# Kernel tuning notes

Measured on AMD Instinct MI355X. Metric: run time of the kernel, lower is better.

## Reference

```python
import jax, jax.numpy as jnp
import numpy as np

# Clause structure: 4 unary clauses and 4 binary (joined-space) clauses,
# each with 3 literals; first literal negated ('n' prefix).
U_IDX = np.array([[0, 1, 2], [3, 4, 5], [6, 7, 8], [9, 10, 11]], dtype=np.int32)
U_SIGNS = np.array([[-1.0, 1.0, 1.0]] * 4, dtype=np.float32)
# Joined matrix columns: [u[i1] (0..15), u[i2] (16..31), binary (32..35)]
B_IDX = np.array([[0, 16, 32], [1, 17, 33], [2, 18, 34], [3, 19, 35]], dtype=np.int32)
B_SIGNS = np.array([[-1.0, 1.0, 1.0]] * 4, dtype=np.float32)

N_NODES, N_UNARY = 50000, 16
N_EDGES, N_BINARY = 1600000, 4
INIT_W = 0.5


def setup_inputs() -> dict:
    key = jax.random.key(0)
    k1, k2, k3, k4 = jax.random.split(key, 4)
    unary = jax.random.normal(k1, (N_NODES, N_UNARY), dtype=jnp.float32)
    binary = jax.random.normal(k2, (N_EDGES, N_BINARY), dtype=jnp.float32)
    edge_index = jax.random.randint(k3, (2, N_EDGES), 0, N_NODES, dtype=jnp.int32)
    wu = jnp.full((4,), INIT_W, dtype=jnp.float32)  # learnable unary clause weights
    wb = jnp.full((4,), INIT_W, dtype=jnp.float32)  # learnable binary clause weights
    return {"unary": unary, "binary": binary, "wu": wu, "wb": wb, "edge_index": edge_index}


def _knowledge_enhancer(x, idx, signs, w):
    """x: [R, P]; idx/signs: [C, L]; w: [C]. Returns summed deltas [R, P]."""
    lit = x[:, idx] * signs                                    # [R, C, L] signed literals
    d = (w[:, None] * jax.nn.softmax(lit, axis=-1)) * signs    # [R, C, L] signed deltas
    return jnp.zeros_like(x).at[:, idx].add(d)                 # scatter-sum over clauses


def reference(unary, binary, wu, wb, edge_index):
    i1, i2 = edge_index[0], edge_index[1]
    P = unary.shape[1]
    # Unary knowledge enhancement
    u = unary + _knowledge_enhancer(unary, U_IDX, U_SIGNS, wu)
    # Join: per-edge [u[i1] | u[i2] | binary]
    joined = jnp.concatenate([u[i1], u[i2], binary], axis=1)   # [E, 2P+B]
    d = _knowledge_enhancer(joined, B_IDX, B_SIGNS, wb)        # [E, 2P+B]
    # GroupBy: scatter node blocks back, keep binary block
    n = unary.shape[0]
    delta_up = (jax.ops.segment_sum(d[:, :P], i1, num_segments=n)
                + jax.ops.segment_sum(d[:, P:2 * P], i2, num_segments=n))
    delta_bp = d[:, 2 * P:]
    # activation = identity (default)
    return u + delta_up, binary + delta_bp
```

## Files before the change

### kernel.cpp

```cpp
#include <hip/hip_runtime.h>
#include <hip/hip_bf16.h>

#define N_NODES 50000
#define N_UNARY 16
#define N_EDGES 1600000
#define N_BINARY 4

typedef float vfloat4 __attribute__((ext_vector_type(4)));

#define FP_SCALE 127.0f
#define FP_INV   (1.0f / 127.0f)

#define BUCKET_SHIFT 11
#define BUCKET_NODES 2048
#define N_BUCKETS 25
#define N_GROUPS 50
#define SEG_CAP 73728
#define N_CHUNKS 10

#define TAILS_STRIDE 16

#define SCAT_BLOCK 512
#define SCAT_EPT 4
#define SCAT_EDGES (SCAT_BLOCK * SCAT_EPT)
#define SCAT_RECS (2 * SCAT_EDGES)

#define SEG_BYTES   ((size_t)N_GROUPS * SEG_CAP * 8)
#define TAILS_BYTES ((size_t)4096)
#define ACC_BYTES   ((size_t)N_NODES * 2 * 8)
#define UE_BYTES    ((size_t)N_NODES * 16)
#define WS_NEEDED   (SEG_BYTES + TAILS_BYTES + ACC_BYTES + UE_BYTES)

__device__ inline void enhance_u4(const float x[6], float wu0, float wu1,
                                  float u[4]) {
    float l0 = -x[0], l1 = x[1], l2 = x[2];
    float m  = fmaxf(l0, fmaxf(l1, l2));
    float e0 = __expf(l0 - m), e1 = __expf(l1 - m), e2 = __expf(l2 - m);
    float inv = 1.0f / (e0 + e1 + e2);
    u[0] = x[0] - wu0 * e0 * inv;
    u[1] = x[1] + wu0 * e1 * inv;
    u[2] = x[2] + wu0 * e2 * inv;
    float l3 = -x[3], l4 = x[4], l5 = x[5];
    float m2 = fmaxf(l3, fmaxf(l4, l5));
    float f0 = __expf(l3 - m2), f1 = __expf(l4 - m2), f2 = __expf(l5 - m2);
    float inv2 = 1.0f / (f0 + f1 + f2);
    u[3] = x[3] - wu1 * f0 * inv2;
}

__device__ inline void edge_math(const float* unary, const float* binary,
                                 float wu0, float wu1, const float wc[4],
                                 int i1, int i2, int e,
                                 float s0[4], float s1[4],
                                 float* out_b) {
    const float4* u1p = (const float4*)(unary + (size_t)i1 * N_UNARY);
    const float4* u2p = (const float4*)(unary + (size_t)i2 * N_UNARY);
    float4 x1a = u1p[0], x1b = u1p[1];
    float4 x2a = u2p[0], x2b = u2p[1];
    float xa[6] = {x1a.x, x1a.y, x1a.z, x1a.w, x1b.x, x1b.y};
    float xb[6] = {x2a.x, x2a.y, x2a.z, x2a.w, x2b.x, x2b.y};
    float a[4], b[4];
    enhance_u4(xa, wu0, wu1, a);
    enhance_u4(xb, wu0, wu1, b);

    vfloat4 bn = __builtin_nontemporal_load((const vfloat4*)binary + e);
    float bb[4] = {bn.x, bn.y, bn.z, bn.w};
    float ob[4];
#pragma unroll
    for (int c = 0; c < 4; ++c) {
        float l0 = -a[c], l1 = b[c], l2 = bb[c];
        float m  = fmaxf(l0, fmaxf(l1, l2));
        float e0 = __expf(l0 - m);
        float e1 = __expf(l1 - m);
        float e2 = __expf(l2 - m);
        float inv = 1.0f / (e0 + e1 + e2);
        s0[c] = e0 * inv;
        s1[c] = e1 * inv;
        ob[c] = bb[c] + wc[c] * e2 * inv;
    }
    vfloat4 obv = {ob[0], ob[1], ob[2], ob[3]};
    __builtin_nontemporal_store(obv, (vfloat4*)out_b + e);
}

__device__ inline unsigned long long make_rec(const float s[4], int local_id) {
    unsigned v0 = __float2uint_rn(s[0] * FP_SCALE);
    unsigned v1 = __float2uint_rn(s[1] * FP_SCALE);
    unsigned v2 = __float2uint_rn(s[2] * FP_SCALE);
    unsigned v3 = __float2uint_rn(s[3] * FP_SCALE);
    unsigned pl = v0 | (v1 << 7) | (v2 << 14) | (v3 << 21);
    return (unsigned long long)pl | ((unsigned long long)(unsigned)local_id << 28);
}

__device__ inline unsigned long long pack4_16(const float s[4]) {
    unsigned long long a = __float2uint_rn(s[0] * FP_SCALE);
    unsigned long long b = __float2uint_rn(s[1] * FP_SCALE);
    unsigned long long c = __float2uint_rn(s[2] * FP_SCALE);
    unsigned long long d = __float2uint_rn(s[3] * FP_SCALE);
    return a | (b << 16) | (c << 32) | (d << 48);
}

__global__ void __launch_bounds__(256)
kenn_pre_kernel(const float* __restrict__ unary,
                const float* __restrict__ wu,
                float4* __restrict__ ue,
                unsigned* __restrict__ tails,
                unsigned long long* __restrict__ accN,
                unsigned long long* __restrict__ accP) {
    int n = blockIdx.x * blockDim.x + threadIdx.x;
    if (n < N_GROUPS) tails[n * TAILS_STRIDE] = 0u;
    if (n >= N_NODES) return;
    accN[n] = 0ull;
    accP[n] = 0ull;
    const float4* up = (const float4*)(unary + (size_t)n * N_UNARY);
    float4 x0 = up[0], x1 = up[1];
    float x[6] = {x0.x, x0.y, x0.z, x0.w, x1.x, x1.y};
    float u[4];
    enhance_u4(x, wu[0], wu[1], u);
    ue[n] = make_float4(u[0], u[1], u[2], u[3]);
}

__global__ void __launch_bounds__(SCAT_BLOCK, 8)
kenn_edge_scatter_kernel(const float4* __restrict__ ue,
                         const float* __restrict__ binary,
                         const float* __restrict__ wb,
                         const int* __restrict__ edge_index,
                         unsigned long long* __restrict__ segs,
                         unsigned* __restrict__ tails,
                         float* __restrict__ out_b) {
    __shared__ unsigned l_cnt[N_GROUPS];
    __shared__ unsigned l_pref[N_GROUPS + 1];
    __shared__ unsigned l_gbase[N_GROUPS];
    __shared__ unsigned long long staged[SCAT_RECS];
    __shared__ unsigned char staged_g[SCAT_RECS];

    int tid = threadIdx.x;
    if (tid < N_GROUPS) l_cnt[tid] = 0;
    __syncthreads();

    int base = blockIdx.x * SCAT_EDGES;
    float wc[4] = {wb[0], wb[1], wb[2], wb[3]};

    bool valid[SCAT_EPT];
    unsigned posg1[SCAT_EPT], posg2[SCAT_EPT];
    unsigned long long rec1[SCAT_EPT], rec2[SCAT_EPT];

#pragma unroll
    for (int k = 0; k < SCAT_EPT; ++k) {
        int e = base + k * SCAT_BLOCK + tid;
        valid[k] = (e < N_EDGES);
        if (!valid[k]) continue;
        int i1 = __builtin_nontemporal_load(edge_index + e);
        int i2 = __builtin_nontemporal_load(edge_index + N_EDGES + e);

        float4 av = ue[i1];
        float4 bv = ue[i2];
        float a[4] = {av.x, av.y, av.z, av.w};
        float b[4] = {bv.x, bv.y, bv.z, bv.w};
        vfloat4 bn = __builtin_nontemporal_load((const vfloat4*)binary + e);
        float bb[4] = {bn.x, bn.y, bn.z, bn.w};

        float s0[4], s1[4], ob[4];
#pragma unroll
        for (int c = 0; c < 4; ++c) {
            float l0 = -a[c], l1 = b[c], l2 = bb[c];
            float m  = fmaxf(l0, fmaxf(l1, l2));
            float e0 = __expf(l0 - m);
            float e1 = __expf(l1 - m);
            float e2 = __expf(l2 - m);
            float inv = 1.0f / (e0 + e1 + e2);
            s0[c] = e0 * inv;
            s1[c] = e1 * inv;
            ob[c] = bb[c] + wc[c] * e2 * inv;
        }
        vfloat4 obv = {ob[0], ob[1], ob[2], ob[3]};
        __builtin_nontemporal_store(obv, (vfloat4*)out_b + e);

        rec1[k] = make_rec(s0, i1 & (BUCKET_NODES - 1));
        rec2[k] = make_rec(s1, i2 & (BUCKET_NODES - 1));
        unsigned g1 = (unsigned)(i1 >> BUCKET_SHIFT);
        unsigned g2 = N_BUCKETS + (unsigned)(i2 >> BUCKET_SHIFT);
        unsigned p1 = atomicAdd(&l_cnt[g1], 1u);
        unsigned p2 = atomicAdd(&l_cnt[g2], 1u);
        posg1[k] = (p1 << 6) | g1;
        posg2[k] = (p2 << 6) | g2;
    }
    __syncthreads();

    if (tid < 64) {
        unsigned c = (tid < N_GROUPS) ? l_cnt[tid] : 0u;
        unsigned s = c;
#pragma unroll
        for (int off = 1; off < 64; off <<= 1) {
            unsigned o = __shfl_up(s, off, 64);
            if (tid >= off) s += o;
        }
        if (tid < N_GROUPS) l_pref[tid] = s - c;
        if (tid == N_GROUPS - 1) l_pref[N_GROUPS] = s;
    } else if (tid >= 64 && tid < 64 + N_GROUPS) {
        int g = tid - 64;
        unsigned c = l_cnt[g];
        l_gbase[g] = c ? atomicAdd(tails + g * TAILS_STRIDE, c) : 0u;
    }
    __syncthreads();

#pragma unroll
    for (int k = 0; k < SCAT_EPT; ++k) {
        if (!valid[k]) continue;
        unsigned g1 = posg1[k] & 63u, p1 = l_pref[g1] + (posg1[k] >> 6);
        unsigned g2 = posg2[k] & 63u, p2 = l_pref[g2] + (posg2[k] >> 6);
        staged[p1] = rec1[k];  staged_g[p1] = (unsigned char)g1;
        staged[p2] = rec2[k];  staged_g[p2] = (unsigned char)g2;
    }
    __syncthreads();

    unsigned total = l_pref[N_GROUPS];
    for (unsigned i = tid; i < total; i += SCAT_BLOCK) {
        unsigned g = staged_g[i];
        unsigned long long rec = staged[i];
        unsigned p = l_gbase[g] + (i - l_pref[g]);
        if (p < SEG_CAP)
            __builtin_nontemporal_store(rec, segs + (size_t)g * SEG_CAP + p);
    }
}

__global__ void __launch_bounds__(512)
kenn_reduce_kernel(const unsigned long long* __restrict__ segs,
                   const unsigned* __restrict__ tails,
                   unsigned long long* __restrict__ accN,
                   unsigned long long* __restrict__ accP) {
    __shared__ unsigned long long lacc[BUCKET_NODES];
    int chunk = blockIdx.x;
    int g     = blockIdx.y;
    int tid   = threadIdx.x;

    for (int i = tid; i < BUCKET_NODES; i += blockDim.x) lacc[i] = 0ull;
    __syncthreads();

    unsigned cnt = tails[g * TAILS_STRIDE];
    if (cnt > SEG_CAP) cnt = SEG_CAP;
    unsigned csz   = (cnt + N_CHUNKS - 1) / N_CHUNKS;
    unsigned start = chunk * csz;
    unsigned end   = start + csz;
    if (end > cnt) end = cnt;

    const unsigned long long* seg = segs + (size_t)g * SEG_CAP;
    for (unsigned i = start + tid; i < end; i += blockDim.x) {
        unsigned long long r = seg[i];
        unsigned id = (unsigned)(r >> 28) & (BUCKET_NODES - 1);
        unsigned pl = (unsigned)r & 0x0FFFFFFFu;
        unsigned long long exp =
            (unsigned long long)(pl & 127u) |
            ((unsigned long long)(pl & (127u << 7))  << 9)  |
            ((unsigned long long)(pl & (127u << 14)) << 18) |
            ((unsigned long long)(pl & (127u << 21)) << 27);
        atomicAdd(&lacc[id], exp);
    }
    __syncthreads();

    int bucket = (g < N_BUCKETS) ? g : (g - N_BUCKETS);
    unsigned long long* acc =
        ((g < N_BUCKETS) ? accN : accP) + (size_t)bucket * BUCKET_NODES;
    for (int i = tid; i < BUCKET_NODES; i += blockDim.x) {
        unsigned long long v = lacc[i];
        if (v) atomicAdd(acc + i, v);
    }
}

__global__ void kenn_node_final_kernel(const float* __restrict__ unary,
                                       const float* __restrict__ wu,
                                       const float* __restrict__ wb,
                                       const unsigned long long* __restrict__ accN,
                                       const unsigned long long* __restrict__ accP,
                                       float* __restrict__ out_u) {
    int node = blockIdx.x * blockDim.x + threadIdx.x;
    if (node >= N_NODES) return;

    const float4* up = (const float4*)(unary + (size_t)node * N_UNARY);
    float4 x0 = up[0], x1 = up[1], x2 = up[2], x3 = up[3];
    float x[16] = {x0.x, x0.y, x0.z, x0.w,
                   x1.x, x1.y, x1.z, x1.w,
                   x2.x, x2.y, x2.z, x2.w,
                   x3.x, x3.y, x3.z, x3.w};
    float wuc[4] = {wu[0], wu[1], wu[2], wu[3]};

    float y[16];
#pragma unroll
    for (int i = 0; i < 16; ++i) y[i] = x[i];

#pragma unroll
    for (int c = 0; c < 4; ++c) {
        float l0 = -x[3 * c + 0];
        float l1 =  x[3 * c + 1];
        float l2 =  x[3 * c + 2];
        float m  = fmaxf(l0, fmaxf(l1, l2));
        float e0 = __expf(l0 - m);
        float e1 = __expf(l1 - m);
        float e2 = __expf(l2 - m);
        float inv = 1.0f / (e0 + e1 + e2);
        y[3 * c + 0] -= wuc[c] * e0 * inv;
        y[3 * c + 1] += wuc[c] * e1 * inv;
        y[3 * c + 2] += wuc[c] * e2 * inv;
    }

    unsigned long long pn = accN[node];
    unsigned long long pp = accP[node];

    float wbc[4] = {wb[0], wb[1], wb[2], wb[3]};
    y[0] += wbc[0] * ((float)(int)((pp      ) & 0xffff) - (float)(int)((pn      ) & 0xffff)) * FP_INV;
    y[1] += wbc[1] * ((float)(int)((pp >> 16) & 0xffff) - (float)(int)((pn >> 16) & 0xffff)) * FP_INV;
    y[2] += wbc[2] * ((float)(int)((pp >> 32) & 0xffff) - (float)(int)((pn >> 32) & 0xffff)) * FP_INV;
    y[3] += wbc[3] * ((float)(int)((pp >> 48) & 0xffff) - (float)(int)((pn >> 48) & 0xffff)) * FP_INV;

    float4* op = (float4*)(out_u + (size_t)node * N_UNARY);
    op[0] = make_float4(y[0],  y[1],  y[2],  y[3]);
    op[1] = make_float4(y[4],  y[5],  y[6],  y[7]);
    op[2] = make_float4(y[8],  y[9],  y[10], y[11]);
    op[3] = make_float4(y[12], y[13], y[14], y[15]);
}

__global__ void kenn_edge_atomic_kernel(const float* __restrict__ unary,
                                        const float* __restrict__ binary,
                                        const float* __restrict__ wu,
                                        const float* __restrict__ wb,
                                        const int* __restrict__ edge_index,
                                        unsigned long long* __restrict__ accN,
                                        unsigned long long* __restrict__ accP,
                                        float* __restrict__ out_b) {
    int e = blockIdx.x * blockDim.x + threadIdx.x;
    if (e >= N_EDGES) return;
    int i1 = __builtin_nontemporal_load(edge_index + e);
    int i2 = __builtin_nontemporal_load(edge_index + N_EDGES + e);
    float wu0 = wu[0], wu1 = wu[1];
    float wc[4] = {wb[0], wb[1], wb[2], wb[3]};
    float s0[4], s1[4];
    edge_math(unary, binary, wu0, wu1, wc, i1, i2, e, s0, s1, out_b);
    atomicAdd(accN + i1, pack4_16(s0));
    atomicAdd(accP + i2, pack4_16(s1));
}

extern "C" void kernel_launch(void* const* d_in, const int* in_sizes, int n_in,
                              void* d_out, int out_size, void* d_ws, size_t ws_size,
                              hipStream_t stream) {
    const float* unary      = (const float*)d_in[0];
    const float* binary     = (const float*)d_in[1];
    const float* wu         = (const float*)d_in[2];
    const float* wb         = (const float*)d_in[3];
    const int*   edge_index = (const int*)d_in[4];

    float* out_u = (float*)d_out;
    float* out_b = (float*)d_out + (size_t)N_NODES * N_UNARY;

    if (ws_size >= WS_NEEDED) {
        unsigned long long* segs = (unsigned long long*)d_ws;
        unsigned* tails = (unsigned*)((char*)d_ws + SEG_BYTES);
        unsigned long long* accN =
            (unsigned long long*)((char*)d_ws + SEG_BYTES + TAILS_BYTES);
        unsigned long long* accP = accN + N_NODES;
        float4* ue =
            (float4*)((char*)d_ws + SEG_BYTES + TAILS_BYTES + ACC_BYTES);

        {
            dim3 grid((N_NODES + 255) / 256);
            kenn_pre_kernel<<<grid, dim3(256), 0, stream>>>(
                unary, wu, ue, tails, accN, accP);
        }
        {
            dim3 grid((N_EDGES + SCAT_EDGES - 1) / SCAT_EDGES);
            kenn_edge_scatter_kernel<<<grid, dim3(SCAT_BLOCK), 0, stream>>>(
                ue, binary, wb, edge_index, segs, tails, out_b);
        }
        {
            dim3 grid(N_CHUNKS, N_GROUPS);
            kenn_reduce_kernel<<<grid, dim3(512), 0, stream>>>(
                segs, tails, accN, accP);
        }
        {
            dim3 block(256);
            dim3 grid((N_NODES + 255) / 256);
            kenn_node_final_kernel<<<grid, block, 0, stream>>>(
                unary, wu, wb, accN, accP, out_u);
        }
    } else {
        unsigned long long* accN = (unsigned long long*)d_ws;
        unsigned long long* accP = accN + N_NODES;
        (void)hipMemsetAsync(accN, 0,
                             (size_t)N_NODES * 2 * sizeof(unsigned long long),
                             stream);
        {
            dim3 block(256);
            dim3 grid((N_EDGES + 255) / 256);
            kenn_edge_atomic_kernel<<<grid, block, 0, stream>>>(
                unary, binary, wu, wb, edge_index, accN, accP, out_b);
        }
        {
            dim3 block(256);
            dim3 grid((N_NODES + 255) / 256);
            kenn_node_final_kernel<<<grid, block, 0, stream>>>(
                unary, wu, wb, accN, accP, out_u);
        }
    }
}
```

Baseline: 150.7 us.

## Fuse four-stage pipeline into one cooperative persistent kernel with grid syncs

Replaces the four separate launches (node pre-pass, edge scatter, bucket reduce, node finalize) with a single cooperative kernel that walks through the phases separated by grid.sync, using an atomic work counter to hand out edge tiles dynamically. The aim is to remove inter-kernel launch gaps and tail effects. The cost is grid-wide barriers, a grid capped at 512 blocks, and smaller per-block tiles. The fallback path now uses 1024-thread scatter blocks.

After: 361.3 us. 2.4x slower.

```diff
diff --git a/kernel.cpp b/kernel.cpp
--- a/kernel.cpp
+++ b/kernel.cpp
@@ -1,5 +1,8 @@
 #include <hip/hip_runtime.h>
 #include <hip/hip_bf16.h>
+#include <hip/hip_cooperative_groups.h>
+
+namespace cg = cooperative_groups;
 
 #define N_NODES 50000
 #define N_UNARY 16
@@ -19,11 +22,20 @@
 #define N_CHUNKS 10
 
 #define TAILS_STRIDE 16
-
-#define SCAT_BLOCK 512
-#define SCAT_EPT 4
-#define SCAT_EDGES (SCAT_BLOCK * SCAT_EPT)
+#define WORK_IDX 1023
+
+#define FUSE_BLOCK 512
+#define FUSE_MAX_GRID 512
+
+#define SCAT_EPT 2
+#define SCAT_EDGES (FUSE_BLOCK * SCAT_EPT)
 #define SCAT_RECS (2 * SCAT_EDGES)
+#define N_TILES ((N_EDGES + SCAT_EDGES - 1) / SCAT_EDGES)
+
+#define SCAT2_BLOCK 1024
+#define SCAT2_EPT 2
+#define SCAT2_EDGES (SCAT2_BLOCK * SCAT2_EPT)
+#define SCAT2_RECS (2 * SCAT2_EDGES)
 
 #define SEG_BYTES   ((size_t)N_GROUPS * SEG_CAP * 8)
 #define TAILS_BYTES ((size_t)4096)
@@ -47,21 +59,32 @@
     u[3] = x[3] - wu1 * f0 * inv2;
 }
 
-__device__ inline void edge_math(const float* unary, const float* binary,
-                                 float wu0, float wu1, const float wc[4],
-                                 int i1, int i2, int e,
+__device__ inline unsigned long long make_rec(const float s[4], int local_id) {
+    unsigned v0 = __float2uint_rn(s[0] * FP_SCALE);
+    unsigned v1 = __float2uint_rn(s[1] * FP_SCALE);
+    unsigned v2 = __float2uint_rn(s[2] * FP_SCALE);
+    unsigned v3 = __float2uint_rn(s[3] * FP_SCALE);
+    unsigned pl = v0 | (v1 << 7) | (v2 << 14) | (v3 << 21);
+    return (unsigned long long)pl | ((unsigned long long)(unsigned)local_id << 28);
+}
+
+__device__ inline unsigned long long pack4_16(const float s[4]) {
+    unsigned long long a = __float2uint_rn(s[0] * FP_SCALE);
+    unsigned long long b = __float2uint_rn(s[1] * FP_SCALE);
+    unsigned long long c = __float2uint_rn(s[2] * FP_SCALE);
+    unsigned long long d = __float2uint_rn(s[3] * FP_SCALE);
+    return a | (b << 16) | (c << 32) | (d << 48);
+}
+
+__device__ inline void edge_core(const float4* __restrict__ ue,
+                                 const float* __restrict__ binary,
+                                 const float wc[4], int i1, int i2, int e,
                                  float s0[4], float s1[4],
-                                 float* out_b) {
-    const float4* u1p = (const float4*)(unary + (size_t)i1 * N_UNARY);
-    const float4* u2p = (const float4*)(unary + (size_t)i2 * N_UNARY);
-    float4 x1a = u1p[0], x1b = u1p[1];
-    float4 x2a = u2p[0], x2b = u2p[1];
-    float xa[6] = {x1a.x, x1a.y, x1a.z, x1a.w, x1b.x, x1b.y};
-    float xb[6] = {x2a.x, x2a.y, x2a.z, x2a.w, x2b.x, x2b.y};
-    float a[4], b[4];
-    enhance_u4(xa, wu0, wu1, a);
-    enhance_u4(xb, wu0, wu1, b);
-
+                                 float* __restrict__ out_b) {
+    float4 av = ue[i1];
+    float4 bv = ue[i2];
+    float a[4] = {av.x, av.y, av.z, av.w};
+    float b[4] = {bv.x, bv.y, bv.z, bv.w};
     vfloat4 bn = __builtin_nontemporal_load((const vfloat4*)binary + e);
     float bb[4] = {bn.x, bn.y, bn.z, bn.w};
     float ob[4];
@@ -81,22 +104,210 @@
     __builtin_nontemporal_store(obv, (vfloat4*)out_b + e);
 }
 
-__device__ inline unsigned long long make_rec(const float s[4], int local_id) {
-    unsigned v0 = __float2uint_rn(s[0] * FP_SCALE);
-    unsigned v1 = __float2uint_rn(s[1] * FP_SCALE);
-    unsigned v2 = __float2uint_rn(s[2] * FP_SCALE);
-    unsigned v3 = __float2uint_rn(s[3] * FP_SCALE);
-    unsigned pl = v0 | (v1 << 7) | (v2 << 14) | (v3 << 21);
-    return (unsigned long long)pl | ((unsigned long long)(unsigned)local_id << 28);
-}
-
-__device__ inline unsigned long long pack4_16(const float s[4]) {
-    unsigned long long a = __float2uint_rn(s[0] * FP_SCALE);
-    unsigned long long b = __float2uint_rn(s[1] * FP_SCALE);
-    unsigned long long c = __float2uint_rn(s[2] * FP_SCALE);
-    unsigned long long d = __float2uint_rn(s[3] * FP_SCALE);
-    return a | (b << 16) | (c << 32) | (d << 48);
-}
+__global__ void __launch_bounds__(FUSE_BLOCK, 4)
+kenn_fused_kernel(const float* __restrict__ unary,
+                  const float* __restrict__ binary,
+                  const float* __restrict__ wu,
+                  const float* __restrict__ wb,
+                  const int* __restrict__ edge_index,
+                  unsigned long long* __restrict__ segs,
+                  unsigned* __restrict__ tails,
+                  unsigned long long* __restrict__ accN,
+                  unsigned long long* __restrict__ accP,
+                  float4* __restrict__ ue,
+                  float* __restrict__ out_u,
+                  float* __restrict__ out_b) {
+    __shared__ unsigned l_cnt[N_GROUPS];
+    __shared__ unsigned l_pref[N_GROUPS + 1];
+    __shared__ unsigned l_gbase[N_GROUPS];
+    __shared__ unsigned long long staged[SCAT_RECS];
+    __shared__ unsigned char staged_g[SCAT_RECS];
+    __shared__ int s_tile;
+
+    cg::grid_group grid = cg::this_grid();
+    const int tid  = threadIdx.x;
+    const int nthr = (int)gridDim.x * FUSE_BLOCK;
+    const int gt0  = (int)blockIdx.x * FUSE_BLOCK + tid;
+
+    for (int n = gt0; n < N_NODES; n += nthr) {
+        if (n < N_GROUPS) tails[n * TAILS_STRIDE] = 0u;
+        if (n == 0) tails[WORK_IDX] = 0u;
+        accN[n] = 0ull;
+        accP[n] = 0ull;
+        const float4* up = (const float4*)(unary + (size_t)n * N_UNARY);
+        float4 x0 = up[0], x1 = up[1];
+        float x[6] = {x0.x, x0.y, x0.z, x0.w, x1.x, x1.y};
+        float u[4];
+        enhance_u4(x, wu[0], wu[1], u);
+        ue[n] = make_float4(u[0], u[1], u[2], u[3]);
+    }
+    __threadfence();
+    grid.sync();
+
+    {
+        float wc[4] = {wb[0], wb[1], wb[2], wb[3]};
+        for (;;) {
+            if (tid == 0) s_tile = (int)atomicAdd(tails + WORK_IDX, 1u);
+            if (tid < N_GROUPS) l_cnt[tid] = 0;
+            __syncthreads();
+            int tile = s_tile;
+            if (tile >= N_TILES) break;
+            int base = tile * SCAT_EDGES;
+
+            bool valid[SCAT_EPT];
+            unsigned posg1[SCAT_EPT], posg2[SCAT_EPT];
+            unsigned long long rec1[SCAT_EPT], rec2[SCAT_EPT];
+
+#pragma unroll
+            for (int k = 0; k < SCAT_EPT; ++k) {
+                int e = base + k * FUSE_BLOCK + tid;
+                valid[k] = (e < N_EDGES);
+                if (!valid[k]) continue;
+                int i1 = __builtin_nontemporal_load(edge_index + e);
+                int i2 = __builtin_nontemporal_load(edge_index + N_EDGES + e);
+                float s0[4], s1[4];
+                edge_core(ue, binary, wc, i1, i2, e, s0, s1, out_b);
+                rec1[k] = make_rec(s0, i1 & (BUCKET_NODES - 1));
+                rec2[k] = make_rec(s1, i2 & (BUCKET_NODES - 1));
+                unsigned g1 = (unsigned)(i1 >> BUCKET_SHIFT);
+                unsigned g2 = N_BUCKETS + (unsigned)(i2 >> BUCKET_SHIFT);
+                unsigned p1 = atomicAdd(&l_cnt[g1], 1u);
+                unsigned p2 = atomicAdd(&l_cnt[g2], 1u);
+                posg1[k] = (p1 << 6) | g1;
+                posg2[k] = (p2 << 6) | g2;
+            }
+            __syncthreads();
+
+            if (tid < 64) {
+                unsigned c = (tid < N_GROUPS) ? l_cnt[tid] : 0u;
+                unsigned s = c;
+#pragma unroll
+                for (int off = 1; off < 64; off <<= 1) {
+                    unsigned o = __shfl_up(s, off, 64);
+                    if (tid >= off) s += o;
+                }
+                if (tid < N_GROUPS) l_pref[tid] = s - c;
+                if (tid == N_GROUPS - 1) l_pref[N_GROUPS] = s;
+            } else if (tid >= 64 && tid < 64 + N_GROUPS) {
+                int g = tid - 64;
+                unsigned c = l_cnt[g];
+                l_gbase[g] = c ? atomicAdd(tails + g * TAILS_STRIDE, c) : 0u;
+            }
+            __syncthreads();
+
+#pragma unroll
+            for (int k = 0; k < SCAT_EPT; ++k) {
+                if (!valid[k]) continue;
+                unsigned g1 = posg1[k] & 63u, p1 = l_pref[g1] + (posg1[k] >> 6);
+                unsigned g2 = posg2[k] & 63u, p2 = l_pref[g2] + (posg2[k] >> 6);
+                staged[p1] = rec1[k];  staged_g[p1] = (unsigned char)g1;
+                staged[p2] = rec2[k];  staged_g[p2] = (unsigned char)g2;
+            }
+            __syncthreads();
+
+            unsigned total = l_pref[N_GROUPS];
+            for (unsigned i = tid; i < total; i += FUSE_BLOCK) {
+                unsigned g = staged_g[i];
+                unsigned long long rec = staged[i];
+                unsigned p = l_gbase[g] + (i - l_pref[g]);
+                if (p < SEG_CAP)
+                    __builtin_nontemporal_store(rec, segs + (size_t)g * SEG_CAP + p);
+            }
+            __syncthreads();
+        }
+    }
+    __threadfence();
+    grid.sync();
+
+    {
+        unsigned long long* lacc = staged;
+        for (int task = blockIdx.x; task < N_GROUPS * N_CHUNKS;
+             task += (int)gridDim.x) {
+            int g     = task / N_CHUNKS;
+            int chunk = task % N_CHUNKS;
+
+            for (int i = tid; i < BUCKET_NODES; i += FUSE_BLOCK) lacc[i] = 0ull;
+            __syncthreads();
+
+            unsigned cnt = tails[g * TAILS_STRIDE];
+            if (cnt > SEG_CAP) cnt = SEG_CAP;
+            unsigned csz   = (cnt + N_CHUNKS - 1) / N_CHUNKS;
+            unsigned start = chunk * csz;
+            unsigned end   = start + csz;
+            if (end > cnt) end = cnt;
+
+            const unsigned long long* seg = segs + (size_t)g * SEG_CAP;
+            for (unsigned i = start + tid; i < end; i += FUSE_BLOCK) {
+                unsigned long long r = seg[i];
+                unsigned id = (unsigned)(r >> 28) & (BUCKET_NODES - 1);
+                unsigned pl = (unsigned)r & 0x0FFFFFFFu;
+                unsigned long long exp =
+                    (unsigned long long)(pl & 127u) |
+                    ((unsigned long long)(pl & (127u << 7))  << 9)  |
+                    ((unsigned long long)(pl & (127u << 14)) << 18) |
+                    ((unsigned long long)(pl & (127u << 21)) << 27);
+                atomicAdd(&lacc[id], exp);
+            }
+            __syncthreads();
+
+            int bucket = (g < N_BUCKETS) ? g : (g - N_BUCKETS);
+            unsigned long long* acc =
+                ((g < N_BUCKETS) ? accN : accP) + (size_t)bucket * BUCKET_NODES;
+            for (int i = tid; i < BUCKET_NODES; i += FUSE_BLOCK) {
+                unsigned long long v = lacc[i];
+                if (v) atomicAdd(acc + i, v);
+            }
+            __syncthreads();
+        }
+    }
+    __threadfence();
+    grid.sync();
+
+    for (int node = gt0; node < N_NODES; node += nthr) {
+        const float4* up = (const float4*)(unary + (size_t)node * N_UNARY);
+        float4 x0 = up[0], x1 = up[1], x2 = up[2], x3 = up[3];
+        float x[16] = {x0.x, x0.y, x0.z, x0.w,
+                       x1.x, x1.y, x1.z, x1.w,
+                       x2.x, x2.y, x2.z, x2.w,
+                       x3.x, x3.y, x3.z, x3.w};
+        float wuc[4] = {wu[0], wu[1], wu[2], wu[3]};
+
+        float y[16];
+#pragma unroll
+        for (int i = 0; i < 16; ++i) y[i] = x[i];
+
+#pragma unroll
+        for (int c = 0; c < 4; ++c) {
+            float l0 = -x[3 * c + 0];
+            float l1 =  x[3 * c + 1];
+            float l2 =  x[3 * c + 2];
+            float m  = fmaxf(l0, fmaxf(l1, l2));
+            float e0 = __expf(l0 - m);
+            float e1 = __expf(l1 - m);
+            float e2 = __expf(l2 - m);
+            float inv = 1.0f / (e0 + e1 + e2);
+            y[3 * c + 0] -= wuc[c] * e0 * inv;
+            y[3 * c + 1] += wuc[c] * e1 * inv;
+            y[3 * c + 2] += wuc[c] * e2 * inv;
+        }
+
+        unsigned long long pn = accN[node];
+        unsigned long long pp = accP[node];
+
+        float wbc[4] = {wb[0], wb[1], wb[2], wb[3]};
+        y[0] += wbc[0] * ((float)(int)((pp      ) & 0xffff) - (float)(int)((pn      ) & 0xffff)) * FP_INV;
+        y[1] += wbc[1] * ((float)(int)((pp >> 16) & 0xffff) - (float)(int)((pn >> 16) & 0xffff)) * FP_INV;
+        y[2] += wbc[2] * ((float)(int)((pp >> 32) & 0xffff) - (float)(int)((pn >> 32) & 0xffff)) * FP_INV;
+        y[3] += wbc[3] * ((float)(int)((pp >> 48) & 0xffff) - (float)(int)((pn >> 48) & 0xffff)) * FP_INV;
+
+        float4* op = (float4*)(out_u + (size_t)node * N_UNARY);
+        op[0] = make_float4(y[0],  y[1],  y[2],  y[3]);
+        op[1] = make_float4(y[4],  y[5],  y[6],  y[7]);
+        op[2] = make_float4(y[8],  y[9],  y[10], y[11]);
+        op[3] = make_float4(y[12], y[13], y[14], y[15]);
+    }
+}
+
 
 __global__ void __launch_bounds__(256)
 kenn_pre_kernel(const float* __restrict__ unary,
@@ -118,7 +329,7 @@
     ue[n] = make_float4(u[0], u[1], u[2], u[3]);
 }
 
-__global__ void __launch_bounds__(SCAT_BLOCK, 8)
+__global__ void __launch_bounds__(SCAT2_BLOCK)
 kenn_edge_scatter_kernel(const float4* __restrict__ ue,
                          const float* __restrict__ binary,
                          const float* __restrict__ wb,
@@ -129,51 +340,29 @@
     __shared__ unsigned l_cnt[N_GROUPS];
     __shared__ unsigned l_pref[N_GROUPS + 1];
     __shared__ unsigned l_gbase[N_GROUPS];
-    __shared__ unsigned long long staged[SCAT_RECS];
-    __shared__ unsigned char staged_g[SCAT_RECS];
+    __shared__ unsigned long long staged[SCAT2_RECS];
+    __shared__ unsigned char staged_g[SCAT2_RECS];
 
     int tid = threadIdx.x;
     if (tid < N_GROUPS) l_cnt[tid] = 0;
     __syncthreads();
 
-    int base = blockIdx.x * SCAT_EDGES;
+    int base = blockIdx.x * SCAT2_EDGES;
     float wc[4] = {wb[0], wb[1], wb[2], wb[3]};
 
-    bool valid[SCAT_EPT];
-    unsigned posg1[SCAT_EPT], posg2[SCAT_EPT];
-    unsigned long long rec1[SCAT_EPT], rec2[SCAT_EPT];
-
-#pragma unroll
-    for (int k = 0; k < SCAT_EPT; ++k) {
-        int e = base + k * SCAT_BLOCK + tid;
+    bool valid[SCAT2_EPT];
+    unsigned posg1[SCAT2_EPT], posg2[SCAT2_EPT];
+    unsigned long long rec1[SCAT2_EPT], rec2[SCAT2_EPT];
+
+#pragma unroll
+    for (int k = 0; k < SCAT2_EPT; ++k) {
+        int e = base + k * SCAT2_BLOCK + tid;
         valid[k] = (e < N_EDGES);
         if (!valid[k]) continue;
         int i1 = __builtin_nontemporal_load(edge_index + e);
         int i2 = __builtin_nontemporal_load(edge_index + N_EDGES + e);
-
-        float4 av = ue[i1];
-        float4 bv = ue[i2];
-        float a[4] = {av.x, av.y, av.z, av.w};
-        float b[4] = {bv.x, bv.y, bv.z, bv.w};
-        vfloat4 bn = __builtin_nontemporal_load((const vfloat4*)binary + e);
-        float bb[4] = {bn.x, bn.y, bn.z, bn.w};
-
-        float s0[4], s1[4], ob[4];
-#pragma unroll
-        for (int c = 0; c < 4; ++c) {
-            float l0 = -a[c], l1 = b[c], l2 = bb[c];
-            float m  = fmaxf(l0, fmaxf(l1, l2));
-            float e0 = __expf(l0 - m);
-            float e1 = __expf(l1 - m);
-            float e2 = __expf(l2 - m);
-            float inv = 1.0f / (e0 + e1 + e2);
-            s0[c] = e0 * inv;
-            s1[c] = e1 * inv;
-            ob[c] = bb[c] + wc[c] * e2 * inv;
-        }
-        vfloat4 obv = {ob[0], ob[1], ob[2], ob[3]};
-        __builtin_nontemporal_store(obv, (vfloat4*)out_b + e);
-
+        float s0[4], s1[4];
+        edge_core(ue, binary, wc, i1, i2, e, s0, s1, out_b);
         rec1[k] = make_rec(s0, i1 & (BUCKET_NODES - 1));
         rec2[k] = make_rec(s1, i2 & (BUCKET_NODES - 1));
         unsigned g1 = (unsigned)(i1 >> BUCKET_SHIFT);
@@ -203,7 +392,7 @@
     __syncthreads();
 
 #pragma unroll
-    for (int k = 0; k < SCAT_EPT; ++k) {
+    for (int k = 0; k < SCAT2_EPT; ++k) {
         if (!valid[k]) continue;
         unsigned g1 = posg1[k] & 63u, p1 = l_pref[g1] + (posg1[k] >> 6);
         unsigned g2 = posg2[k] & 63u, p2 = l_pref[g2] + (posg2[k] >> 6);
@@ -213,7 +402,7 @@
     __syncthreads();
 
     unsigned total = l_pref[N_GROUPS];
-    for (unsigned i = tid; i < total; i += SCAT_BLOCK) {
+    for (unsigned i = tid; i < total; i += SCAT2_BLOCK) {
         unsigned g = staged_g[i];
         unsigned long long rec = staged[i];
         unsigned p = l_gbase[g] + (i - l_pref[g]);
@@ -331,11 +520,40 @@
     int i2 = __builtin_nontemporal_load(edge_index + N_EDGES + e);
     float wu0 = wu[0], wu1 = wu[1];
     float wc[4] = {wb[0], wb[1], wb[2], wb[3]};
-    float s0[4], s1[4];
-    edge_math(unary, binary, wu0, wu1, wc, i1, i2, e, s0, s1, out_b);
+
+    const float4* u1p = (const float4*)(unary + (size_t)i1 * N_UNARY);
+    const float4* u2p = (const float4*)(unary + (size_t)i2 * N_UNARY);
+    float4 x1a = u1p[0], x1b = u1p[1];
+    float4 x2a = u2p[0], x2b = u2p[1];
+    float xa[6] = {x1a.x, x1a.y, x1a.z, x1a.w, x1b.x, x1b.y};
+    float xb[6] = {x2a.x, x2a.y, x2a.z, x2a.w, x2b.x, x2b.y};
+    float a[4], b[4];
+    enhance_u4(xa, wu0, wu1, a);
+    enhance_u4(xb, wu0, wu1, b);
+
+    vfloat4 bn = __builtin_nontemporal_load((const vfloat4*)binary + e);
+    float bb[4] = {bn.x, bn.y, bn.z, bn.w};
+    float s0[4], s1[4], ob[4];
+#pragma unroll
+    for (int c = 0; c < 4; ++c) {
+        float l0 = -a[c], l1 = b[c], l2 = bb[c];
+        float m  = fmaxf(l0, fmaxf(l1, l2));
+        float e0 = __expf(l0 - m);
+        float e1 = __expf(l1 - m);
+        float e2 = __expf(l2 - m);
+        float inv = 1.0f / (e0 + e1 + e2);
+        s0[c] = e0 * inv;
+        s1[c] = e1 * inv;
+        ob[c] = bb[c] + wc[c] * e2 * inv;
+    }
+    vfloat4 obv = {ob[0], ob[1], ob[2], ob[3]};
+    __builtin_nontemporal_store(obv, (vfloat4*)out_b + e);
+
     atomicAdd(accN + i1, pack4_16(s0));
     atomicAdd(accP + i2, pack4_16(s1));
 }
+
+static int g_coop_grid = -1;
 
 extern "C" void kernel_launch(void* const* d_in, const int* in_sizes, int n_in,
                               void* d_out, int out_size, void* d_ws, size_t ws_size,
@@ -358,26 +576,56 @@
         float4* ue =
             (float4*)((char*)d_ws + SEG_BYTES + TAILS_BYTES + ACC_BYTES);
 
-        {
-            dim3 grid((N_NODES + 255) / 256);
-            kenn_pre_kernel<<<grid, dim3(256), 0, stream>>>(
-                unary, wu, ue, tails, accN, accP);
-        }
-        {
-            dim3 grid((N_EDGES + SCAT_EDGES - 1) / SCAT_EDGES);
-            kenn_edge_scatter_kernel<<<grid, dim3(SCAT_BLOCK), 0, stream>>>(
-                ue, binary, wb, edge_index, segs, tails, out_b);
-        }
-        {
-            dim3 grid(N_CHUNKS, N_GROUPS);
-            kenn_reduce_kernel<<<grid, dim3(512), 0, stream>>>(
-                segs, tails, accN, accP);
-        }
-        {
-            dim3 block(256);
-            dim3 grid((N_NODES + 255) / 256);
-            kenn_node_final_kernel<<<grid, block, 0, stream>>>(
-                unary, wu, wb, accN, accP, out_u);
+        if (g_coop_grid < 0) {
+            int nb = 0;
+            hipError_t oe = hipOccupancyMaxActiveBlocksPerMultiprocessor(
+                &nb, (const void*)kenn_fused_kernel, FUSE_BLOCK, 0);
+            if (oe != hipSuccess || nb < 1) {
+                g_coop_grid = 0;
+            } else {
+                long g = (long)nb * 256;
+                if (g > FUSE_MAX_GRID) g = FUSE_MAX_GRID;
+                g_coop_grid = (int)g;
+            }
+        }
+
+        bool done = false;
+        if (g_coop_grid > 0) {
+            void* args[] = {
+                (void*)&unary, (void*)&binary, (void*)&wu, (void*)&wb,
+                (void*)&edge_index, (void*)&segs, (void*)&tails,
+                (void*)&accN, (void*)&accP, (void*)&ue,
+                (void*)&out_u, (void*)&out_b
+            };
+            hipError_t le = hipLaunchCooperativeKernel(
+                (const void*)kenn_fused_kernel, dim3(g_coop_grid),
+                dim3(FUSE_BLOCK), args, 0, stream);
+            if (le == hipSuccess) done = true;
+            else g_coop_grid = 0;
+        }
+
+        if (!done) {
+            {
+                dim3 grid((N_NODES + 255) / 256);
+                kenn_pre_kernel<<<grid, dim3(256), 0, stream>>>(
+                    unary, wu, ue, tails, accN, accP);
+            }
+            {
+                dim3 grid((N_EDGES + SCAT2_EDGES - 1) / SCAT2_EDGES);
+                kenn_edge_scatter_kernel<<<grid, dim3(SCAT2_BLOCK), 0, stream>>>(
+                    ue, binary, wb, edge_index, segs, tails, out_b);
+            }
+            {
+                dim3 grid(N_CHUNKS, N_GROUPS);
+                kenn_reduce_kernel<<<grid, dim3(512), 0, stream>>>(
+                    segs, tails, accN, accP);
+            }
+            {
+                dim3 block(256);
+                dim3 grid((N_NODES + 255) / 256);
+                kenn_node_final_kernel<<<grid, block, 0, stream>>>(
+                    unary, wu, wb, accN, accP, out_u);
+            }
         }
     } else {
         unsigned long long* accN = (unsigned long long*)d_ws;
```
